# Optimization experiments

Measured on AMD Instinct MI355X. Metric: run time of the kernel, lower is better.

The kernel has to match this reference:

```python
import jax, jax.numpy as jnp
import numpy as np

B, H, W, C = 8, 64, 64, 512   # C = query_dim = text_dim
K = 256                        # text tokens
TOP_M = 5
EPS = 1e-5


def _ln(x, g, b):
    mu = jnp.mean(x, axis=-1, keepdims=True)
    var = jnp.var(x, axis=-1, keepdims=True)
    return (x - mu) / jnp.sqrt(var + EPS) * g + b


def setup_inputs() -> dict:
    key = jax.random.key(0)
    ks = jax.random.split(key, 10)
    s = 0.02
    return {
        "visual": jax.random.normal(ks[0], (B, H, W, C), jnp.float32),
        "text": jax.random.normal(ks[1], (B, K, C), jnp.float32),
        "g1": jnp.ones((C,), jnp.float32), "b1": jnp.zeros((C,), jnp.float32),
        "g2": jnp.ones((C,), jnp.float32), "b2": jnp.zeros((C,), jnp.float32),
        "Wq": jax.random.normal(ks[2], (C, C), jnp.float32) * s,   # query_dim -> text_dim
        "Wv": jax.random.normal(ks[3], (C, C), jnp.float32) * s,   # text_dim -> query_dim
        "logit_scale": jnp.asarray(np.log(1.0 / 0.07), jnp.float32),
        "Wg": jax.random.normal(ks[4], (C, 1), jnp.float32) * s,
        "bg": jnp.zeros((1,), jnp.float32),
        "W1": jax.random.normal(ks[5], (C, 4 * C), jnp.float32) * s,
        "bff1": jnp.zeros((4 * C,), jnp.float32),
        "W2": jax.random.normal(ks[6], (4 * C, C), jnp.float32) * s,
        "bff2": jnp.zeros((C,), jnp.float32),
    }


def reference(visual, text, g1, b1, g2, b2, Wq, Wv, logit_scale, Wg, bg, W1, bff1, W2, bff2):
    Bv, Hv, Wdim, Cv = visual.shape
    N = Hv * Wdim
    x = _ln(visual, g1, b1).reshape(Bv, N, Cv)           # (B,N,C) pre-LN
    q = x @ Wq                                            # (B,N,Ct)
    q = q / jnp.linalg.norm(q, axis=-1, keepdims=True)
    k = text / jnp.linalg.norm(text, axis=-1, keepdims=True)  # (B,K,Ct)
    v = text @ Wv                                         # (B,K,C)
    scale = jnp.exp(logit_scale) / jnp.sqrt(jnp.asarray(Cv, jnp.float32))
    sim = jnp.einsum('bnc,bkc->bnk', q, k) * scale        # (B,N,K)
    top_vals, top_idx = jax.lax.top_k(sim, TOP_M)         # (B,N,m)
    attn = jax.nn.softmax(top_vals, axis=-1)
    v_sel = jax.vmap(lambda vb, ib: vb[ib])(v, top_idx)   # (B,N,m,C) gather
    aligned = jnp.einsum('bnm,bnmc->bnc', attn, v_sel)    # weighted sum
    gate = jax.nn.sigmoid(x @ Wg + bg)                    # (B,N,1)
    aligned = aligned * gate
    y = x + aligned                                        # residual
    y = _ln(y, g2, b2)
    h = jax.nn.gelu(y @ W1 + bff1, approximate=False)
    y = y + (h @ W2 + bff2)
    return y.reshape(Bv, Hv, Wdim, Cv)
```

## Files before the change

### kernel.cpp

```cpp
#include <hip/hip_runtime.h>
#include <hip/hip_bf16.h>

typedef unsigned short u16;
typedef float f32x4 __attribute__((ext_vector_type(4)));
typedef short bf16x8 __attribute__((ext_vector_type(8)));

#define DEV __device__ __forceinline__

DEV float btof(u16 u) { return __uint_as_float(((unsigned)u) << 16); }
DEV u16 f2b(float f) {
  unsigned u = __float_as_uint(f);
  return (u16)((u + 0x7fffu + ((u >> 16) & 1u)) >> 16);
}
DEV void gld16(const void* g, void* l) {
  __builtin_amdgcn_global_load_lds(
      (const __attribute__((address_space(1))) void*)g,
      (__attribute__((address_space(3))) void*)l, 16, 0, 0);
}
DEV float gelu_fast(float x) {
  float xx = x * x;
  float p = fmaf(xx, -0.10294357f, -2.3022077f);
  float e; asm("v_exp_f32 %0, %1" : "=v"(e) : "v"(p * x));
  float r; asm("v_rcp_f32 %0, %1" : "=v"(r) : "v"(1.0f + e));
  return x * r;
}

template <int EPI, int MR>
__global__ __launch_bounds__(512, 2) void gemm256(
    const u16* __restrict__ A, long lda, const u16* __restrict__ B, long ldb,
    void* __restrict__ Cv, long ldc, int K, long sA, long sB, long sC,
    const float* __restrict__ aux1, const void* __restrict__ aux2)
{
  __shared__ u16 lds[4][MR * 1024 + 8192];
  const int tid = threadIdx.x;
  const int lane = tid & 63, wid = tid >> 6;
  const int wm = wid >> 2, wn = wid & 3;
  const int qr = lane >> 4, qc = lane & 15;

  const int gx = gridDim.x, gy = gridDim.y;
  const int nwg = gx * gy * (int)gridDim.z;
  const int orig = blockIdx.x + gx * (blockIdx.y + gy * blockIdx.z);
  const int nid = (orig & 7) * (nwg >> 3) + (orig >> 3);
  const int bx = nid % gx;
  const int rem1 = nid / gx;
  const int by = rem1 % gy;
  const long z = rem1 / gy;

  const long m0 = (long)by * (MR * 32), n0 = (long)bx << 8;
  const u16* Ab = A + z * sA;
  const u16* Bb = B + z * sB;
  const int T = K >> 5;

  f32x4 acc[MR][4];
#pragma unroll
  for (int m = 0; m < MR; ++m)
#pragma unroll
    for (int n = 0; n < 4; ++n) acc[m][n] = (f32x4){0.f, 0.f, 0.f, 0.f};

  const int cb0 = wid * 128 + lane, cb1 = cb0 + 64;
  const int rb0 = cb0 >> 2, rb1 = cb1 >> 2;
  const int kb0off = ((cb0 & 3) ^ ((rb0 >> 1) & 3)) << 3;
  const int kb1off = ((cb1 & 3) ^ ((rb1 >> 1) & 3)) << 3;
  const u16* pb0 = Bb + (n0 + rb0) * ldb + kb0off;
  const u16* pb1 = Bb + (n0 + rb1) * ldb + kb1off;
  const int eb0 = cb0 * 8, eb1 = cb1 * 8;

  const int ca0 = (MR == 8) ? (wid * 128 + lane) : (wid * 64 + lane);
  const int ca1 = ca0 + 64;
  const int ra0 = ca0 >> 2, ra1 = ca1 >> 2;
  const int ka0off = ((ca0 & 3) ^ ((ra0 >> 1) & 3)) << 3;
  const int ka1off = ((ca1 & 3) ^ ((ra1 >> 1) & 3)) << 3;
  const u16* pa0 = Ab + (m0 + ra0) * lda + ka0off;
  const u16* pa1 = (MR == 8) ? (Ab + (m0 + ra1) * lda + ka1off) : pa0;
  const int ea0 = ca0 * 8, ea1 = ca1 * 8;

  const int swz = (qr ^ ((qc >> 1) & 3)) << 3;

  auto stageA = [&](int bsel, int so) {
    gld16(pa0 + so, &lds[bsel][ea0]);
    if constexpr (MR == 8) gld16(pa1 + so, &lds[bsel][ea1]);
  };
  auto stageB = [&](int bsel, int so) {
    gld16(pb0 + so, &lds[bsel][MR * 1024 + eb0]);
    gld16(pb1 + so, &lds[bsel][MR * 1024 + eb1]);
  };
  auto ldA4 = [&](bf16x8* dst, int bsel, int mh) {
#pragma unroll
    for (int mm = 0; mm < 4; ++mm) {
      const int rr = wm * (MR * 16) + (mh * 4 + mm) * 16 + qc;
      dst[mm] = *(const bf16x8*)&lds[bsel][rr * 32 + swz];
    }
  };
  auto ldB4 = [&](bf16x8* dst, int bsel) {
#pragma unroll
    for (int n = 0; n < 4; ++n) {
      const int rr = wn * 64 + n * 16 + qc;
      dst[n] = *(const bf16x8*)&lds[bsel][MR * 1024 + rr * 32 + swz];
    }
  };

  stageA(0, 0);  stageB(0, 0);
  stageA(1, 32); stageB(1, 32);
  pa0 += 64; pa1 += 64; pb0 += 64; pb1 += 64;

#define WAITV(N) asm volatile("s_waitcnt vmcnt(" #N ")" ::: "memory")
#define MFMAQ(MB) \
    __builtin_amdgcn_s_setprio(1); \
    _Pragma("unroll") \
    for (int mm = 0; mm < 4; ++mm) \
      _Pragma("unroll") \
      for (int n = 0; n < 4; ++n) \
        acc[MB + mm][n] = __builtin_amdgcn_mfma_f32_16x16x32_bf16( \
            a4[mm], b4[n], acc[MB + mm][n], 0, 0, 0); \
    __builtin_amdgcn_s_setprio(0);

#define TILE32(BUF, PF1, PF2, SO) { \
    bf16x8 a4[4], b4[4]; \
    if (PF2) { stageA((BUF + 2) & 3, SO); stageB((BUF + 2) & 3, SO); \
               if constexpr (MR == 8) { WAITV(8); } else { WAITV(6); } } \
    else if (PF1) { if constexpr (MR == 8) { WAITV(4); } else { WAITV(3); } } \
    else { WAITV(0); } \
    __builtin_amdgcn_s_barrier(); \
    ldA4(a4, BUF, 0); ldB4(b4, BUF); \
    MFMAQ(0) \
    if constexpr (MR == 8) { \
      ldA4(a4, BUF, 1); \
      MFMAQ(4) \
    } \
    asm volatile("s_waitcnt lgkmcnt(0)" ::: "memory"); \
    __builtin_amdgcn_s_barrier(); }

  for (int t2 = 0; t2 < T; t2 += 4) {
    const bool pfn = (t2 + 4 < T);
    TILE32(0, true, true, 0)
    TILE32(1, true, true, 32)
    TILE32(2, true, pfn, 64)
    TILE32(3, pfn, pfn, 96)
    pa0 += 128; pa1 += 128; pb0 += 128; pb1 += 128;
  }
#undef TILE32
#undef MFMAQ
#undef WAITV

  if constexpr (EPI == 6) {
    float* rsc2 = (float*)Cv;
#pragma unroll
    for (int m = 0; m < MR; ++m)
#pragma unroll
      for (int j = 0; j < 4; ++j) {
        float s = 0.f;
#pragma unroll
        for (int n = 0; n < 4; ++n) { float t2 = acc[m][n][j]; s = fmaf(t2, t2, s); }
        s += __shfl_xor(s, 1); s += __shfl_xor(s, 2);
        s += __shfl_xor(s, 4); s += __shfl_xor(s, 8);
        if (qc == 0)
          atomicAdd(rsc2 + (m0 + wm * (MR * 16) + m * 16 + qr * 4 + j), s);
      }
  } else {
#pragma unroll
    for (int m = 0; m < MR; ++m) {
#pragma unroll
      for (int n = 0; n < 4; ++n) {
        const long row0 = m0 + wm * (MR * 16) + m * 16 + qr * 4;
        const long col = n0 + wn * 64 + n * 16 + qc;
#pragma unroll
        for (int j = 0; j < 4; ++j) {
          const long idx = z * sC + (row0 + j) * ldc + col;
          float val = acc[m][n][j];
          if constexpr (EPI == 0) ((float*)Cv)[idx] = val;
          else if constexpr (EPI == 4)
            ((u16*)Cv)[idx] = f2b(gelu_fast(val + aux1[col]));
          else if constexpr (EPI == 5) {
            float r = btof(((const u16*)aux2)[idx]);
            ((float*)Cv)[idx] = val + aux1[col] + r;
          }
        }
      }
    }
  }
}

template <int EPI>
__global__ __launch_bounds__(256) void gemm_bt(
    const u16* __restrict__ A, long lda, const u16* __restrict__ B, long ldb,
    void* __restrict__ Cv, long ldc, int K)
{
  const int tid = threadIdx.x;
  const int lane = tid & 63, wv = tid >> 6;
  const int wr = wv >> 1, wc = wv & 1;
  const int m0 = blockIdx.y << 7, n0 = blockIdx.x << 7;

  __shared__ u16 lsA[128 * 64];
  __shared__ u16 lsB[128 * 64];

  f32x4 acc[4][4];
#pragma unroll
  for (int m = 0; m < 4; ++m)
#pragma unroll
    for (int n = 0; n < 4; ++n) acc[m][n] = (f32x4){0.f, 0.f, 0.f, 0.f};

  const int srow = tid >> 3;
  const int scol = (tid & 7) << 3;
  const int qr = lane >> 4, qc = lane & 15;

  for (int k0 = 0; k0 < K; k0 += 64) {
#pragma unroll
    for (int p = 0; p < 4; ++p) {
      gld16(A + (long)(m0 + (p << 5) + srow) * lda + k0 + scol,
            &lsA[(p * 4 + wv) * 512]);
      gld16(B + (long)(n0 + (p << 5) + srow) * ldb + k0 + scol,
            &lsB[(p * 4 + wv) * 512]);
    }
    __syncthreads();
#pragma unroll
    for (int kk = 0; kk < 64; kk += 32) {
      bf16x8 af[4], bfr[4];
#pragma unroll
      for (int m = 0; m < 4; ++m)
        af[m] = *(const bf16x8*)&lsA[(wr * 64 + m * 16 + qc) * 64 + kk + qr * 8];
#pragma unroll
      for (int n = 0; n < 4; ++n)
        bfr[n] = *(const bf16x8*)&lsB[(wc * 64 + n * 16 + qc) * 64 + kk + qr * 8];
#pragma unroll
      for (int m = 0; m < 4; ++m)
#pragma unroll
        for (int n = 0; n < 4; ++n)
          acc[m][n] = __builtin_amdgcn_mfma_f32_16x16x32_bf16(af[m], bfr[n],
                                                              acc[m][n], 0, 0, 0);
    }
    __syncthreads();
  }

#pragma unroll
  for (int m = 0; m < 4; ++m) {
#pragma unroll
    for (int n = 0; n < 4; ++n) {
      const int row0 = m0 + wr * 64 + m * 16 + qr * 4;
      const int col = n0 + wc * 64 + n * 16 + qc;
#pragma unroll
      for (int j = 0; j < 4; ++j) {
        const long idx = (long)(row0 + j) * ldc + col;
        if constexpr (EPI == 3) ((u16*)Cv)[idx] = f2b(acc[m][n][j]);
      }
    }
  }
}

__global__ __launch_bounds__(256) void prep_kernel(
    const float* __restrict__ vis, const float* __restrict__ text,
    const float* __restrict__ g1, const float* __restrict__ b1,
    const float* __restrict__ Wg, const float* __restrict__ bg,
    const float* __restrict__ Wq, const float* __restrict__ Wv,
    const float* __restrict__ W1, const float* __restrict__ W2,
    u16* __restrict__ x3, u16* __restrict__ xr2, float* __restrict__ gate,
    float* __restrict__ kT, u16* __restrict__ tb,
    u16* __restrict__ WqT, u16* __restrict__ WvT,
    u16* __restrict__ W1T, u16* __restrict__ W2T, float* __restrict__ rsc2)
{
  const int bid = blockIdx.x;
  const int lane = threadIdx.x & 63, wv = threadIdx.x >> 6;

  if (bid < 640) {
    const float* src; u16* dst; int R, C, id, tilesX;
    if (bid < 64)       { src = Wq; dst = WqT; R = 512;  C = 512;  id = bid;       tilesX = 8; }
    else if (bid < 128) { src = Wv; dst = WvT; R = 512;  C = 512;  id = bid - 64;  tilesX = 8; }
    else if (bid < 384) { src = W1; dst = W1T; R = 512;  C = 2048; id = bid - 128; tilesX = 32; }
    else                { src = W2; dst = W2T; R = 2048; C = 512;  id = bid - 384; tilesX = 8; }
    const int c0 = (id % tilesX) * 64, r0 = (id / tilesX) * 64;
    __shared__ float t[64][65];
    const int tx = threadIdx.x & 63, ty = threadIdx.x >> 6;
    for (int j = ty; j < 64; j += 4)
      t[j][tx] = src[(long)(r0 + j) * C + c0 + tx];
    __syncthreads();
    for (int j = ty; j < 64; j += 4)
      dst[(long)(c0 + j) * R + r0 + tx] = f2b(t[tx][j]);
    return;
  }

  if (bid < 8832) {
    const long row = (long)(bid - 640) * 4 + wv;
    const float* src = vis + row * 512 + lane * 8;
    float v[8];
    *(float4*)&v[0] = *(const float4*)src;
    *(float4*)&v[4] = *(const float4*)(src + 4);
    float s = 0.f, sq = 0.f;
#pragma unroll
    for (int j = 0; j < 8; ++j) { s += v[j]; sq += v[j] * v[j]; }
#pragma unroll
    for (int off = 32; off; off >>= 1) { s += __shfl_xor(s, off); sq += __shfl_xor(sq, off); }
    const float mu = s * (1.f / 512.f);
    const float var = sq * (1.f / 512.f) - mu * mu;
    const float rstd = 1.0f / sqrtf(var + 1e-5f);

    float g1r[8], b1r[8], wgr[8];
    *(float4*)&g1r[0] = *(const float4*)(g1 + lane * 8);
    *(float4*)&g1r[4] = *(const float4*)(g1 + lane * 8 + 4);
    *(float4*)&b1r[0] = *(const float4*)(b1 + lane * 8);
    *(float4*)&b1r[4] = *(const float4*)(b1 + lane * 8 + 4);
    *(float4*)&wgr[0] = *(const float4*)(Wg + lane * 8);
    *(float4*)&wgr[4] = *(const float4*)(Wg + lane * 8 + 4);

    bf16x8 p0, p1, p2;
    float gd = 0.f;
#pragma unroll
    for (int j = 0; j < 8; ++j) {
      float d = (v[j] - mu) * rstd * g1r[j] + b1r[j];
      gd += d * wgr[j];
      u16 h0 = f2b(d);        float r1 = d - btof(h0);
      u16 h1 = f2b(r1);       float r2 = r1 - btof(h1);
      u16 h2 = f2b(r2);
      p0[j] = (short)h0; p1[j] = (short)h1; p2[j] = (short)h2;
    }
#pragma unroll
    for (int off = 32; off; off >>= 1) gd += __shfl_xor(gd, off);
    if (lane == 0) gate[row] = 1.0f / (1.0f + __expf(-(gd + bg[0])));

    u16* dst = x3 + row * 1536 + lane * 8;
    *(bf16x8*)dst = p0;
    *(bf16x8*)(dst + 512) = p1;
    *(bf16x8*)(dst + 1024) = p0;
    *(bf16x8*)(xr2 + row * 512 + lane * 8) = p2;
    return;
  }

  if (bid < 9344) {
    const long row = (long)(bid - 8832) * 4 + wv;
    const int b = (int)(row >> 8), tok = (int)(row & 255);
    const float* src = text + row * 512 + lane * 8;
    float v[8];
    *(float4*)&v[0] = *(const float4*)src;
    *(float4*)&v[4] = *(const float4*)(src + 4);
    float sq = 0.f;
#pragma unroll
    for (int j = 0; j < 8; ++j) sq += v[j] * v[j];
#pragma unroll
    for (int off = 32; off; off >>= 1) sq += __shfl_xor(sq, off);
    const float inv = 1.0f / sqrtf(sq);
    bf16x8 pt;
    float* kdst = kT + (long)b * 131072 + tok;
#pragma unroll
    for (int j = 0; j < 8; ++j) {
      kdst[(long)(lane * 8 + j) * 256] = v[j] * inv;
      pt[j] = (short)f2b(v[j]);
    }
    *(bf16x8*)(tb + row * 512 + lane * 8) = pt;
    return;
  }

  rsc2[threadIdx.x] = 0.f;
  rsc2[256 + threadIdx.x] = 0.f;
}

__global__ __launch_bounds__(256) void wtilde_kernel(
    const float* __restrict__ Wq, const float* __restrict__ kT,
    u16* __restrict__ wA, double* __restrict__ wtmpT)
{
  const int c0 = blockIdx.x * 4;
  const int b = blockIdx.y;
  __shared__ float wrow[4][512];
#pragma unroll
  for (int i = 0; i < 8; ++i) {
    int idx = threadIdx.x + i * 256;
    wrow[idx >> 9][idx & 511] = Wq[(long)c0 * 512 + idx];
  }
  __syncthreads();
  const int k = threadIdx.x;
  const float* kTb = kT + (long)b * 131072 + k;
  double a[4] = {0, 0, 0, 0};
  for (int j = 0; j < 512; ++j) {
    double kvd = (double)kTb[(long)j * 256];
    a[0] += (double)wrow[0][j] * kvd;
    a[1] += (double)wrow[1][j] * kvd;
    a[2] += (double)wrow[2][j] * kvd;
    a[3] += (double)wrow[3][j] * kvd;
  }
  const long kb = (long)b * 256 + k;
#pragma unroll
  for (int i = 0; i < 4; ++i) {
    const int c = c0 + i;
    u16 h0 = f2b((float)a[i]);  double r1 = a[i] - (double)btof(h0);
    u16 h1 = f2b((float)r1);
    wA[kb * 1536 + c] = h0;
    wA[kb * 1536 + 512 + c] = h0;
    wA[kb * 1536 + 1024 + c] = h1;
    wtmpT[kb * 512 + c] = a[i];
  }
}

__global__ __launch_bounds__(256) void topk_fuse(
    const float* __restrict__ sim, const u16* __restrict__ v,
    const u16* __restrict__ x3, const u16* __restrict__ xr2,
    const float* __restrict__ gate, const double* __restrict__ wtmpT,
    const float* __restrict__ rsc2, const float* __restrict__ ls,
    const float* __restrict__ g2, const float* __restrict__ b2,
    u16* __restrict__ yb)
{
  const int lane = threadIdx.x & 63, wv = threadIdx.x >> 6;
  const long row = (long)blockIdx.x * 4 + wv;
  const int b = (int)(row >> 12);

  const u16* xr = x3 + row * 1536 + lane * 8;
  bf16x8 a0 = *(const bf16x8*)xr;
  bf16x8 a1 = *(const bf16x8*)(xr + 512);
  float xv[8];
#pragma unroll
  for (int j = 0; j < 8; ++j) xv[j] = btof((u16)a0[j]) + btof((u16)a1[j]);

  float4 sv = *(const float4*)(sim + row * 256 + lane * 4);
  float vals[4] = {sv.x, sv.y, sv.z, sv.w};
  float topv[8]; int topi[8];
#pragma unroll
  for (int m = 0; m < 8; ++m) {
    float bv = vals[0]; int bl = 0;
    if (vals[1] > bv) { bv = vals[1]; bl = 1; }
    if (vals[2] > bv) { bv = vals[2]; bl = 2; }
    if (vals[3] > bv) { bv = vals[3]; bl = 3; }
    int bi = lane * 4 + bl;
#pragma unroll
    for (int off = 32; off; off >>= 1) {
      float ov = __shfl_xor(bv, off);
      int oi = __shfl_xor(bi, off);
      if (ov > bv || (ov == bv && oi < bi)) { bv = ov; bi = oi; }
    }
    topv[m] = bv; topi[m] = bi;
    if ((bi >> 2) == lane) {
      int tt = bi & 3;
      if (tt == 0) vals[0] = -INFINITY; else if (tt == 1) vals[1] = -INFINITY;
      else if (tt == 2) vals[2] = -INFINITY; else vals[3] = -INFINITY;
    }
  }

  if (topv[4] - topv[5] < 2e-4f) {
    bf16x8 a2 = *(const bf16x8*)(xr2 + row * 512 + lane * 8);
    double xd[8];
#pragma unroll
    for (int j = 0; j < 8; ++j)
      xd[j] = (double)btof((u16)a0[j]) + (double)btof((u16)a1[j]) +
              (double)btof((u16)a2[j]);
    double cv[8]; int ti[8];
#pragma unroll
    for (int m = 0; m < 8; ++m) {
      const double* wp = wtmpT + ((long)b * 256 + topi[m]) * 512 + lane * 8;
      double a = 0.0;
#pragma unroll
      for (int j = 0; j < 8; ++j) a += xd[j] * wp[j];
#pragma unroll
      for (int off = 32; off; off >>= 1) a += __shfl_xor(a, off);
      cv[m] = a; ti[m] = topi[m];
    }
#define CE(i, jj) { \
    bool sw = (cv[jj] > cv[i]) || (cv[jj] == cv[i] && ti[jj] < ti[i]); \
    double tv = cv[i]; int tix = ti[i]; \
    cv[i] = sw ? cv[jj] : cv[i];  ti[i] = sw ? ti[jj] : ti[i]; \
    cv[jj] = sw ? tv : cv[jj];    ti[jj] = sw ? tix : ti[jj]; }
    CE(0,1) CE(2,3) CE(4,5) CE(6,7)
    CE(0,2) CE(1,3) CE(4,6) CE(5,7)
    CE(1,2) CE(5,6)
    CE(0,4) CE(1,5) CE(2,6) CE(3,7)
    CE(2,4) CE(3,5)
    CE(1,2) CE(3,4) CE(5,6)
#undef CE
#pragma unroll
    for (int m = 0; m < 5; ++m) { topv[m] = (float)cv[m]; topi[m] = ti[m]; }
  }

  const float rs = __expf(ls[0]) * 0.044194173824159223f * rsqrtf(rsc2[row]);
  float e[5], se = 0.f;
#pragma unroll
  for (int m = 0; m < 5; ++m) {
    e[m] = __expf((topv[m] - topv[0]) * rs); se += e[m];
  }
  const float inv = 1.0f / se;
  const float g = gate[row];

  float acc8[8] = {0, 0, 0, 0, 0, 0, 0, 0};
#pragma unroll
  for (int m = 0; m < 5; ++m) {
    const u16* vr = v + ((long)b * 256 + topi[m]) * 512 + lane * 8;
    bf16x8 vv = *(const bf16x8*)vr;
    float wgt = e[m] * inv;
#pragma unroll
    for (int j = 0; j < 8; ++j) acc8[j] += wgt * btof((u16)vv[j]);
  }

  float y8[8]; float s = 0.f, sq = 0.f;
#pragma unroll
  for (int j = 0; j < 8; ++j) {
    y8[j] = xv[j] + acc8[j] * g;
    s += y8[j]; sq += y8[j] * y8[j];
  }
#pragma unroll
  for (int off = 32; off; off >>= 1) { s += __shfl_xor(s, off); sq += __shfl_xor(sq, off); }
  const float mu = s * (1.f / 512.f);
  const float var = sq * (1.f / 512.f) - mu * mu;
  const float rstd = 1.0f / sqrtf(var + 1e-5f);

  float g2r[8], b2r[8];
  *(float4*)&g2r[0] = *(const float4*)(g2 + lane * 8);
  *(float4*)&g2r[4] = *(const float4*)(g2 + lane * 8 + 4);
  *(float4*)&b2r[0] = *(const float4*)(b2 + lane * 8);
  *(float4*)&b2r[4] = *(const float4*)(b2 + lane * 8 + 4);
  bf16x8 outp;
#pragma unroll
  for (int j = 0; j < 8; ++j)
    outp[j] = (short)f2b((y8[j] - mu) * rstd * g2r[j] + b2r[j]);
  *(bf16x8*)(yb + row * 512 + lane * 8) = outp;
}

extern "C" void kernel_launch(void* const* d_in, const int* in_sizes, int n_in,
                              void* d_out, int out_size, void* d_ws,
                              size_t ws_size, hipStream_t stream)
{
  const float* vis  = (const float*)d_in[0];
  const float* text = (const float*)d_in[1];
  const float* g1   = (const float*)d_in[2];
  const float* b1   = (const float*)d_in[3];
  const float* g2   = (const float*)d_in[4];
  const float* b2   = (const float*)d_in[5];
  const float* Wq   = (const float*)d_in[6];
  const float* Wv   = (const float*)d_in[7];
  const float* ls   = (const float*)d_in[8];
  const float* Wg   = (const float*)d_in[9];
  const float* bg   = (const float*)d_in[10];
  const float* W1   = (const float*)d_in[11];
  const float* bff1 = (const float*)d_in[12];
  const float* W2   = (const float*)d_in[13];
  const float* bff2 = (const float*)d_in[14];
  (void)in_sizes; (void)n_in; (void)out_size; (void)ws_size;

  char* w = (char*)d_ws;
  auto alloc = [&](size_t bytes) {
    char* p = w; w += (bytes + 255) & ~(size_t)255; return p;
  };
  u16* x3 = (u16*)alloc(134217728);
  u16* h = x3;
  char* gap = (char*)x3 + 100663296;
  double* wtmpT = (double*)gap;
  u16* wA = (u16*)(gap + 8388608);
  float* sim = (float*)alloc(33554432);
  u16* yb = (u16*)alloc(33554432);
  u16* xr2 = (u16*)alloc(33554432);
  float* kT = (float*)alloc(4194304);
  u16* tb = (u16*)alloc(2097152);
  u16* vb = (u16*)alloc(2097152);
  u16* WqT = (u16*)alloc(524288);
  u16* WvT = (u16*)alloc(524288);
  u16* W1T = (u16*)alloc(2097152);
  u16* W2T = (u16*)alloc(2097152);
  float* gate = (float*)alloc(131072);
  float* rsc2 = (float*)alloc(131072);

  dim3 b256(256), b512(512);

  prep_kernel<<<9345, b256, 0, stream>>>(vis, text, g1, b1, Wg, bg, Wq, Wv,
                                         W1, W2, x3, xr2, gate, kT, tb, WqT,
                                         WvT, W1T, W2T, rsc2);

  wtilde_kernel<<<dim3(128, 8), b256, 0, stream>>>(Wq, kT, wA, wtmpT);

  gemm256<6, 8><<<dim3(2, 128, 1), b512, 0, stream>>>(
      x3, 1536, WqT, 512, rsc2, 1, 512, 0, 0, 0, nullptr, nullptr);

  gemm_bt<3><<<dim3(4, 16, 1), b256, 0, stream>>>(tb, 512, WvT, 512, vb, 512,
                                                  512);

  gemm256<0, 4><<<dim3(1, 32, 8), b512, 0, stream>>>(
      x3, 1536, wA, 1536, sim, 256, 1536, 4096L * 1536, 256L * 1536,
      4096L * 256, nullptr, nullptr);

  topk_fuse<<<8192, b256, 0, stream>>>(sim, vb, x3, xr2, gate, wtmpT, rsc2,
                                       ls, g2, b2, yb);

  gemm256<4, 8><<<dim3(8, 128, 1), b512, 0, stream>>>(
      yb, 512, W1T, 512, h, 2048, 512, 0, 0, 0, bff1, nullptr);
  gemm256<5, 8><<<dim3(2, 128, 1), b512, 0, stream>>>(
      h, 2048, W2T, 2048, d_out, 512, 2048, 0, 0, 0, bff2, yb);
}
```

Measured before the change: 402.5 us.

## Use single-bf16 similarity GEMM with wider exact-rescore candidate window

The similarity GEMM previously ran over a three-term split-bf16 expansion (K=1536) to approximate fp32 precision. It now uses only the leading bf16 term (K=512), and the q-projection GEMM is pointed at that same single-term buffer. To keep top-5 selection correct, top_k now extracts 10 candidates and the fp64 rescoring fallback fires under a looser gap threshold (8e-3 instead of 2e-4). The cost is more rows taking the slower double-precision rescore path, plus a risk of wrong selections when the true top-5 falls outside the bf16 top-10.

New measurement: 422.0 us. +4.8%, slower.

```diff
diff --git a/kernel.cpp b/kernel.cpp
--- a/kernel.cpp
+++ b/kernel.cpp
@@ -252,7 +252,7 @@
     const float* __restrict__ Wg, const float* __restrict__ bg,
     const float* __restrict__ Wq, const float* __restrict__ Wv,
     const float* __restrict__ W1, const float* __restrict__ W2,
-    u16* __restrict__ x3, u16* __restrict__ xr2, float* __restrict__ gate,
+    u16* __restrict__ x0b, u16* __restrict__ xr12, float* __restrict__ gate,
     float* __restrict__ kT, u16* __restrict__ tb,
     u16* __restrict__ WqT, u16* __restrict__ WvT,
     u16* __restrict__ W1T, u16* __restrict__ W2T, float* __restrict__ rsc2)
@@ -315,11 +315,10 @@
     for (int off = 32; off; off >>= 1) gd += __shfl_xor(gd, off);
     if (lane == 0) gate[row] = 1.0f / (1.0f + __expf(-(gd + bg[0])));
 
-    u16* dst = x3 + row * 1536 + lane * 8;
-    *(bf16x8*)dst = p0;
-    *(bf16x8*)(dst + 512) = p1;
-    *(bf16x8*)(dst + 1024) = p0;
-    *(bf16x8*)(xr2 + row * 512 + lane * 8) = p2;
+    *(bf16x8*)(x0b + row * 512 + lane * 8) = p0;
+    u16* dst = xr12 + row * 1024 + lane * 8;
+    *(bf16x8*)dst = p1;
+    *(bf16x8*)(dst + 512) = p2;
     return;
   }
 
@@ -378,18 +377,14 @@
 #pragma unroll
   for (int i = 0; i < 4; ++i) {
     const int c = c0 + i;
-    u16 h0 = f2b((float)a[i]);  double r1 = a[i] - (double)btof(h0);
-    u16 h1 = f2b((float)r1);
-    wA[kb * 1536 + c] = h0;
-    wA[kb * 1536 + 512 + c] = h0;
-    wA[kb * 1536 + 1024 + c] = h1;
+    wA[kb * 512 + c] = f2b((float)a[i]);
     wtmpT[kb * 512 + c] = a[i];
   }
 }
 
 __global__ __launch_bounds__(256) void topk_fuse(
     const float* __restrict__ sim, const u16* __restrict__ v,
-    const u16* __restrict__ x3, const u16* __restrict__ xr2,
+    const u16* __restrict__ x0b, const u16* __restrict__ xr12,
     const float* __restrict__ gate, const double* __restrict__ wtmpT,
     const float* __restrict__ rsc2, const float* __restrict__ ls,
     const float* __restrict__ g2, const float* __restrict__ b2,
@@ -399,18 +394,17 @@
   const long row = (long)blockIdx.x * 4 + wv;
   const int b = (int)(row >> 12);
 
-  const u16* xr = x3 + row * 1536 + lane * 8;
-  bf16x8 a0 = *(const bf16x8*)xr;
-  bf16x8 a1 = *(const bf16x8*)(xr + 512);
+  bf16x8 a0 = *(const bf16x8*)(x0b + row * 512 + lane * 8);
+  bf16x8 a1 = *(const bf16x8*)(xr12 + row * 1024 + lane * 8);
   float xv[8];
 #pragma unroll
   for (int j = 0; j < 8; ++j) xv[j] = btof((u16)a0[j]) + btof((u16)a1[j]);
 
   float4 sv = *(const float4*)(sim + row * 256 + lane * 4);
   float vals[4] = {sv.x, sv.y, sv.z, sv.w};
-  float topv[8]; int topi[8];
-#pragma unroll
-  for (int m = 0; m < 8; ++m) {
+  float topv[10]; int topi[10];
+#pragma unroll
+  for (int m = 0; m < 10; ++m) {
     float bv = vals[0]; int bl = 0;
     if (vals[1] > bv) { bv = vals[1]; bl = 1; }
     if (vals[2] > bv) { bv = vals[2]; bl = 2; }
@@ -430,16 +424,16 @@
     }
   }
 
-  if (topv[4] - topv[5] < 2e-4f) {
-    bf16x8 a2 = *(const bf16x8*)(xr2 + row * 512 + lane * 8);
+  if (topv[4] - topv[5] < 8e-3f) {
+    bf16x8 a2 = *(const bf16x8*)(xr12 + row * 1024 + 512 + lane * 8);
     double xd[8];
 #pragma unroll
     for (int j = 0; j < 8; ++j)
       xd[j] = (double)btof((u16)a0[j]) + (double)btof((u16)a1[j]) +
               (double)btof((u16)a2[j]);
-    double cv[8]; int ti[8];
-#pragma unroll
-    for (int m = 0; m < 8; ++m) {
+    double cv[10]; int ti[10];
+#pragma unroll
+    for (int m = 0; m < 10; ++m) {
       const double* wp = wtmpT + ((long)b * 256 + topi[m]) * 512 + lane * 8;
       double a = 0.0;
 #pragma unroll
@@ -448,20 +442,21 @@
       for (int off = 32; off; off >>= 1) a += __shfl_xor(a, off);
       cv[m] = a; ti[m] = topi[m];
     }
-#define CE(i, jj) { \
-    bool sw = (cv[jj] > cv[i]) || (cv[jj] == cv[i] && ti[jj] < ti[i]); \
-    double tv = cv[i]; int tix = ti[i]; \
-    cv[i] = sw ? cv[jj] : cv[i];  ti[i] = sw ? ti[jj] : ti[i]; \
-    cv[jj] = sw ? tv : cv[jj];    ti[jj] = sw ? tix : ti[jj]; }
-    CE(0,1) CE(2,3) CE(4,5) CE(6,7)
-    CE(0,2) CE(1,3) CE(4,6) CE(5,7)
-    CE(1,2) CE(5,6)
-    CE(0,4) CE(1,5) CE(2,6) CE(3,7)
-    CE(2,4) CE(3,5)
-    CE(1,2) CE(3,4) CE(5,6)
-#undef CE
-#pragma unroll
-    for (int m = 0; m < 5; ++m) { topv[m] = (float)cv[m]; topi[m] = ti[m]; }
+    unsigned used = 0;
+#pragma unroll
+    for (int sel = 0; sel < 5; ++sel) {
+      double best = -1e300; int bestTi = 0x7fffffff; int bl = 0;
+#pragma unroll
+      for (int m = 0; m < 10; ++m) {
+        bool ok = ((used >> m) & 1u) == 0u;
+        bool better = ok && (cv[m] > best || (cv[m] == best && ti[m] < bestTi));
+        best = better ? cv[m] : best;
+        bestTi = better ? ti[m] : bestTi;
+        bl = better ? m : bl;
+      }
+      used |= (1u << bl);
+      topv[sel] = (float)best; topi[sel] = bestTi;
+    }
   }
 
   const float rs = __expf(ls[0]) * 0.044194173824159223f * rsqrtf(rsc2[row]);
@@ -532,14 +527,13 @@
   auto alloc = [&](size_t bytes) {
     char* p = w; w += (bytes + 255) & ~(size_t)255; return p;
   };
-  u16* x3 = (u16*)alloc(134217728);
-  u16* h = x3;
-  char* gap = (char*)x3 + 100663296;
-  double* wtmpT = (double*)gap;
-  u16* wA = (u16*)(gap + 8388608);
+  u16* x0b = (u16*)alloc(134217728);
+  u16* h = x0b;
+  u16* xr12 = (u16*)((char*)x0b + 33554432);
+  double* wtmpT = (double*)((char*)x0b + 100663296);
+  u16* wA = (u16*)((char*)x0b + 109051904);
   float* sim = (float*)alloc(33554432);
   u16* yb = (u16*)alloc(33554432);
-  u16* xr2 = (u16*)alloc(33554432);
   float* kT = (float*)alloc(4194304);
   u16* tb = (u16*)alloc(2097152);
   u16* vb = (u16*)alloc(2097152);
@@ -553,22 +547,22 @@
   dim3 b256(256), b512(512);
 
   prep_kernel<<<9345, b256, 0, stream>>>(vis, text, g1, b1, Wg, bg, Wq, Wv,
-                                         W1, W2, x3, xr2, gate, kT, tb, WqT,
+                                         W1, W2, x0b, xr12, gate, kT, tb, WqT,
                                          WvT, W1T, W2T, rsc2);
 
   wtilde_kernel<<<dim3(128, 8), b256, 0, stream>>>(Wq, kT, wA, wtmpT);
 
   gemm256<6, 8><<<dim3(2, 128, 1), b512, 0, stream>>>(
-      x3, 1536, WqT, 512, rsc2, 1, 512, 0, 0, 0, nullptr, nullptr);
+      x0b, 512, WqT, 512, rsc2, 1, 512, 0, 0, 0, nullptr, nullptr);
 
   gemm_bt<3><<<dim3(4, 16, 1), b256, 0, stream>>>(tb, 512, WvT, 512, vb, 512,
                                                   512);
 
   gemm256<0, 4><<<dim3(1, 32, 8), b512, 0, stream>>>(
-      x3, 1536, wA, 1536, sim, 256, 1536, 4096L * 1536, 256L * 1536,
+      x0b, 512, wA, 512, sim, 256, 512, 4096L * 512, 256L * 512,
       4096L * 256, nullptr, nullptr);
 
-  topk_fuse<<<8192, b256, 0, stream>>>(sim, vb, x3, xr2, gate, wtmpT, rsc2,
+  topk_fuse<<<8192, b256, 0, stream>>>(sim, vb, x0b, xr12, gate, wtmpT, rsc2,
                                        ls, g2, b2, yb);
 
   gemm256<4, 8><<<dim3(8, 128, 1), b512, 0, stream>>>(
```

## Merge three independent middle GEMMs into one heterogeneous launch

Applied to the files above, without the earlier changes.

Pulls the GEMM body out into a device function taking an explicit LDS pointer and block coordinates. A new mid_gemms kernel uses one 528-block grid to run the Wq row-norm GEMM, the text@Wv GEMM (moved from the small gemm_bt kernel onto the 256-tile path with a new bf16 epilogue) and the batched sim GEMM. The aim is to cut two kernel launches and the tail gaps between them, letting blocks from independent GEMMs fill the GPU together. The cost is that every block reserves the largest LDS footprint (MR=8), which can lower occupancy for the MR=4 sim blocks.

Measured after the change: 395.8 us (median of 2 runs). Within noise of the previous version (-1.7%).

```diff
diff --git a/kernel.cpp b/kernel.cpp
--- a/kernel.cpp
+++ b/kernel.cpp
@@ -4,6 +4,7 @@
 typedef unsigned short u16;
 typedef float f32x4 __attribute__((ext_vector_type(4)));
 typedef short bf16x8 __attribute__((ext_vector_type(8)));
+typedef __attribute__((address_space(3))) u16 lds_u16;
 
 #define DEV __device__ __forceinline__
 
@@ -12,7 +13,7 @@
   unsigned u = __float_as_uint(f);
   return (u16)((u + 0x7fffu + ((u >> 16) & 1u)) >> 16);
 }
-DEV void gld16(const void* g, void* l) {
+DEV void gld16(const void* g, lds_u16* l) {
   __builtin_amdgcn_global_load_lds(
       (const __attribute__((address_space(1))) void*)g,
       (__attribute__((address_space(3))) void*)l, 16, 0, 0);
@@ -25,26 +26,22 @@
   return x * r;
 }
 
+#define LDSV(p) (*(const __attribute__((address_space(3))) bf16x8*)(p))
+
 template <int EPI, int MR>
-__global__ __launch_bounds__(512, 2) void gemm256(
-    const u16* __restrict__ A, long lda, const u16* __restrict__ B, long ldb,
-    void* __restrict__ Cv, long ldc, int K, long sA, long sB, long sC,
-    const float* __restrict__ aux1, const void* __restrict__ aux2)
-{
-  __shared__ u16 lds[4][MR * 1024 + 8192];
+DEV void gemm_body(lds_u16* LDS, int bx, int by, long z,
+                   const u16* __restrict__ A, long lda,
+                   const u16* __restrict__ B, long ldb,
+                   void* __restrict__ Cv, long ldc, int K,
+                   long sA, long sB, long sC,
+                   const float* __restrict__ aux1,
+                   const void* __restrict__ aux2)
+{
+  constexpr int SLOT = MR * 1024 + 8192;
   const int tid = threadIdx.x;
   const int lane = tid & 63, wid = tid >> 6;
   const int wm = wid >> 2, wn = wid & 3;
   const int qr = lane >> 4, qc = lane & 15;
-
-  const int gx = gridDim.x, gy = gridDim.y;
-  const int nwg = gx * gy * (int)gridDim.z;
-  const int orig = blockIdx.x + gx * (blockIdx.y + gy * blockIdx.z);
-  const int nid = (orig & 7) * (nwg >> 3) + (orig >> 3);
-  const int bx = nid % gx;
-  const int rem1 = nid / gx;
-  const int by = rem1 % gy;
-  const long z = rem1 / gy;
 
   const long m0 = (long)by * (MR * 32), n0 = (long)bx << 8;
   const u16* Ab = A + z * sA;
@@ -77,25 +74,25 @@
   const int swz = (qr ^ ((qc >> 1) & 3)) << 3;
 
   auto stageA = [&](int bsel, int so) {
-    gld16(pa0 + so, &lds[bsel][ea0]);
-    if constexpr (MR == 8) gld16(pa1 + so, &lds[bsel][ea1]);
+    gld16(pa0 + so, LDS + bsel * SLOT + ea0);
+    if constexpr (MR == 8) gld16(pa1 + so, LDS + bsel * SLOT + ea1);
   };
   auto stageB = [&](int bsel, int so) {
-    gld16(pb0 + so, &lds[bsel][MR * 1024 + eb0]);
-    gld16(pb1 + so, &lds[bsel][MR * 1024 + eb1]);
+    gld16(pb0 + so, LDS + bsel * SLOT + MR * 1024 + eb0);
+    gld16(pb1 + so, LDS + bsel * SLOT + MR * 1024 + eb1);
   };
   auto ldA4 = [&](bf16x8* dst, int bsel, int mh) {
 #pragma unroll
     for (int mm = 0; mm < 4; ++mm) {
       const int rr = wm * (MR * 16) + (mh * 4 + mm) * 16 + qc;
-      dst[mm] = *(const bf16x8*)&lds[bsel][rr * 32 + swz];
+      dst[mm] = LDSV(LDS + bsel * SLOT + rr * 32 + swz);
     }
   };
   auto ldB4 = [&](bf16x8* dst, int bsel) {
 #pragma unroll
     for (int n = 0; n < 4; ++n) {
       const int rr = wn * 64 + n * 16 + qc;
-      dst[n] = *(const bf16x8*)&lds[bsel][MR * 1024 + rr * 32 + swz];
+      dst[n] = LDSV(LDS + bsel * SLOT + MR * 1024 + rr * 32 + swz);
     }
   };
 
@@ -168,6 +165,7 @@
           const long idx = z * sC + (row0 + j) * ldc + col;
           float val = acc[m][n][j];
           if constexpr (EPI == 0) ((float*)Cv)[idx] = val;
+          else if constexpr (EPI == 3) ((u16*)Cv)[idx] = f2b(val);
           else if constexpr (EPI == 4)
             ((u16*)Cv)[idx] = f2b(gelu_fast(val + aux1[col]));
           else if constexpr (EPI == 5) {
@@ -180,69 +178,49 @@
   }
 }
 
-template <int EPI>
-__global__ __launch_bounds__(256) void gemm_bt(
+template <int EPI, int MR>
+__global__ __launch_bounds__(512, 2) void gemm256(
     const u16* __restrict__ A, long lda, const u16* __restrict__ B, long ldb,
-    void* __restrict__ Cv, long ldc, int K)
-{
-  const int tid = threadIdx.x;
-  const int lane = tid & 63, wv = tid >> 6;
-  const int wr = wv >> 1, wc = wv & 1;
-  const int m0 = blockIdx.y << 7, n0 = blockIdx.x << 7;
-
-  __shared__ u16 lsA[128 * 64];
-  __shared__ u16 lsB[128 * 64];
-
-  f32x4 acc[4][4];
-#pragma unroll
-  for (int m = 0; m < 4; ++m)
-#pragma unroll
-    for (int n = 0; n < 4; ++n) acc[m][n] = (f32x4){0.f, 0.f, 0.f, 0.f};
-
-  const int srow = tid >> 3;
-  const int scol = (tid & 7) << 3;
-  const int qr = lane >> 4, qc = lane & 15;
-
-  for (int k0 = 0; k0 < K; k0 += 64) {
-#pragma unroll
-    for (int p = 0; p < 4; ++p) {
-      gld16(A + (long)(m0 + (p << 5) + srow) * lda + k0 + scol,
-            &lsA[(p * 4 + wv) * 512]);
-      gld16(B + (long)(n0 + (p << 5) + srow) * ldb + k0 + scol,
-            &lsB[(p * 4 + wv) * 512]);
-    }
-    __syncthreads();
-#pragma unroll
-    for (int kk = 0; kk < 64; kk += 32) {
-      bf16x8 af[4], bfr[4];
-#pragma unroll
-      for (int m = 0; m < 4; ++m)
-        af[m] = *(const bf16x8*)&lsA[(wr * 64 + m * 16 + qc) * 64 + kk + qr * 8];
-#pragma unroll
-      for (int n = 0; n < 4; ++n)
-        bfr[n] = *(const bf16x8*)&lsB[(wc * 64 + n * 16 + qc) * 64 + kk + qr * 8];
-#pragma unroll
-      for (int m = 0; m < 4; ++m)
-#pragma unroll
-        for (int n = 0; n < 4; ++n)
-          acc[m][n] = __builtin_amdgcn_mfma_f32_16x16x32_bf16(af[m], bfr[n],
-                                                              acc[m][n], 0, 0, 0);
-    }
-    __syncthreads();
-  }
-
-#pragma unroll
-  for (int m = 0; m < 4; ++m) {
-#pragma unroll
-    for (int n = 0; n < 4; ++n) {
-      const int row0 = m0 + wr * 64 + m * 16 + qr * 4;
-      const int col = n0 + wc * 64 + n * 16 + qc;
-#pragma unroll
-      for (int j = 0; j < 4; ++j) {
-        const long idx = (long)(row0 + j) * ldc + col;
-        if constexpr (EPI == 3) ((u16*)Cv)[idx] = f2b(acc[m][n][j]);
-      }
-    }
+    void* __restrict__ Cv, long ldc, int K, long sA, long sB, long sC,
+    const float* __restrict__ aux1, const void* __restrict__ aux2)
+{
+  __shared__ u16 lds[4 * (MR * 1024 + 8192)];
+  const int gx = gridDim.x, gy = gridDim.y;
+  const int nwg = gx * gy * (int)gridDim.z;
+  const int orig = blockIdx.x + gx * (blockIdx.y + gy * blockIdx.z);
+  const int nid = (orig & 7) * (nwg >> 3) + (orig >> 3);
+  const int bx = nid % gx;
+  const int rem1 = nid / gx;
+  const int by = rem1 % gy;
+  const long z = rem1 / gy;
+  gemm_body<EPI, MR>((lds_u16*)lds, bx, by, z, A, lda, B, ldb, Cv, ldc, K,
+                     sA, sB, sC, aux1, aux2);
+}
+
+__global__ __launch_bounds__(512, 2) void mid_gemms(
+    const u16* __restrict__ x3, const u16* __restrict__ WqT,
+    float* __restrict__ rsc2, const u16* __restrict__ tb,
+    const u16* __restrict__ WvT, u16* __restrict__ vb,
+    const u16* __restrict__ wA, float* __restrict__ sim)
+{
+  __shared__ u16 slds[4 * (8 * 1024 + 8192)];
+  lds_u16* L = (lds_u16*)slds;
+  const int bid = blockIdx.x;
+  if (bid < 256) {
+    const int nid = ((bid & 7) << 5) + (bid >> 3);
+    gemm_body<6, 8>(L, nid & 1, nid >> 1, 0, x3, 1536, WqT, 512, rsc2, 1,
+                    512, 0, 0, 0, nullptr, nullptr);
+  } else if (bid < 272) {
+    const int l = bid - 256;
+    const int nid = ((l & 7) << 1) + (l >> 3);
+    gemm_body<3, 8>(L, nid & 1, nid >> 1, 0, tb, 512, WvT, 512, vb, 512,
+                    512, 0, 0, 0, nullptr, nullptr);
+  } else {
+    const int l = bid - 272;
+    const int nid = ((l & 7) << 5) + (l >> 3);
+    gemm_body<0, 4>(L, 0, nid & 31, nid >> 5, x3, 1536, wA, 1536, sim, 256,
+                    1536, 4096L * 1536, 256L * 1536, 4096L * 256, nullptr,
+                    nullptr);
   }
 }
 
@@ -558,15 +536,7 @@
 
   wtilde_kernel<<<dim3(128, 8), b256, 0, stream>>>(Wq, kT, wA, wtmpT);
 
-  gemm256<6, 8><<<dim3(2, 128, 1), b512, 0, stream>>>(
-      x3, 1536, WqT, 512, rsc2, 1, 512, 0, 0, 0, nullptr, nullptr);
-
-  gemm_bt<3><<<dim3(4, 16, 1), b256, 0, stream>>>(tb, 512, WvT, 512, vb, 512,
-                                                  512);
-
-  gemm256<0, 4><<<dim3(1, 32, 8), b512, 0, stream>>>(
-      x3, 1536, wA, 1536, sim, 256, 1536, 4096L * 1536, 256L * 1536,
-      4096L * 256, nullptr, nullptr);
+  mid_gemms<<<528, b512, 0, stream>>>(x3, WqT, rsc2, tb, WvT, vb, wA, sim);
 
   topk_fuse<<<8192, b256, 0, stream>>>(sim, vb, x3, xr2, gate, wtmpT, rsc2,
                                        ls, g2, b2, yb);
```
